# Kernel tuning notes

Measured on AMD Instinct MI355X. Metric: run time of the kernel, lower is better.

## Reference

```python
import jax, jax.numpy as jnp
import numpy as np

N_NODES = 50000
N_EDGES = 800000


def _graph_conv(feature, W, b, src, dst, edge_w, n_nodes, activation=None):
    # DGL GraphConv, norm='both', with edge_weight.
    ones = jnp.ones((src.shape[0],), dtype=feature.dtype)
    deg_out = jnp.clip(jax.ops.segment_sum(ones, src, num_segments=n_nodes), 1.0)
    deg_in = jnp.clip(jax.ops.segment_sum(ones, dst, num_segments=n_nodes), 1.0)
    # scale src side by out-deg^-1/2, transform first (in_feats > out_feats path)
    h = (feature * (deg_out ** -0.5)[:, None]) @ W            # [N, out]
    msgs = h[src] * edge_w[:, None]                            # [E, out]
    agg = jax.ops.segment_sum(msgs, dst, num_segments=n_nodes) # [N, out]
    out = agg * (deg_in ** -0.5)[:, None] + b
    if activation is not None:
        out = activation(out)
    return out


def setup_inputs() -> dict:
    key = jax.random.key(0)
    ks = jax.random.split(key, 8)
    feature = jax.random.normal(ks[0], (N_NODES, 768), dtype=jnp.float32)
    src = jax.random.randint(ks[1], (N_EDGES,), 0, N_NODES, dtype=jnp.int32)
    dst = jax.random.randint(ks[2], (N_EDGES,), 0, N_NODES, dtype=jnp.int32)
    edge_w = jax.random.uniform(ks[3], (N_EDGES,), dtype=jnp.float32)
    W1 = jax.random.normal(ks[4], (768, 200), dtype=jnp.float32) * (768 ** -0.5)
    b1 = jnp.zeros((200,), dtype=jnp.float32)
    W2 = jax.random.normal(ks[5], (200, 20), dtype=jnp.float32) * (200 ** -0.5)
    b2 = jnp.zeros((20,), dtype=jnp.float32)
    return {"feature": feature, "src": src, "dst": dst, "edge_w": edge_w,
            "W1": W1, "b1": b1, "W2": W2, "b2": b2}


def reference(feature, src, dst, edge_w, W1, b1, W2, b2):
    n = feature.shape[0]
    # dropout layers are identity in eval mode
    h = _graph_conv(feature, W1, b1, src, dst, edge_w, n, activation=jax.nn.relu)
    out = _graph_conv(h, W2, b2, src, dst, edge_w, n)
    return out
```

## Files before the change

### kernel.cpp

```cpp
#include <hip/hip_runtime.h>

#define N_NODES 50000
#define N_EDGES 800000
#define F_IN 768
#define H1 200
#define H1P 208
#define H2 20
#define NB_SCAN 196
#define NT 13

typedef unsigned short ushort_t;
typedef __attribute__((ext_vector_type(8))) short bf16x8;
typedef __attribute__((ext_vector_type(4))) float f32x4;


__global__ __launch_bounds__(256) void k_count(const int* __restrict__ src,
                                               const int* __restrict__ dst,
                                               int* __restrict__ cnt_src,
                                               int* __restrict__ cnt_dst) {
  int i = blockIdx.x * 256 + threadIdx.x;
  if (i < N_EDGES) {
    atomicAdd(&cnt_src[src[i]], 1);
    atomicAdd(&cnt_dst[dst[i]], 1);
  }
}

__global__ __launch_bounds__(256) void k_scan_block(const int* __restrict__ cnt_dst,
                                                    int* __restrict__ row_start,
                                                    int* __restrict__ partials) {
  __shared__ int sm[256];
  int i = blockIdx.x * 256 + threadIdx.x;
  int v = (i < N_NODES) ? cnt_dst[i] : 0;
  sm[threadIdx.x] = v;
  __syncthreads();
#pragma unroll
  for (int off = 1; off < 256; off <<= 1) {
    int t = (threadIdx.x >= off) ? sm[threadIdx.x - off] : 0;
    __syncthreads();
    sm[threadIdx.x] += t;
    __syncthreads();
  }
  if (i < N_NODES) row_start[i] = sm[threadIdx.x] - v;
  if (threadIdx.x == 255) partials[blockIdx.x] = sm[255];
}

__global__ __launch_bounds__(256) void k_scan_partials(int* __restrict__ partials) {
  __shared__ int sm[256];
  int v = (threadIdx.x < NB_SCAN) ? partials[threadIdx.x] : 0;
  sm[threadIdx.x] = v;
  __syncthreads();
#pragma unroll
  for (int off = 1; off < 256; off <<= 1) {
    int t = (threadIdx.x >= off) ? sm[threadIdx.x - off] : 0;
    __syncthreads();
    sm[threadIdx.x] += t;
    __syncthreads();
  }
  partials[threadIdx.x] = sm[threadIdx.x] - v;
}

__global__ __launch_bounds__(256) void k_scan_add(const int* __restrict__ cnt_dst,
                                                  const int* __restrict__ cnt_src,
                                                  const int* __restrict__ partials,
                                                  int* __restrict__ row_start,
                                                  float* __restrict__ dinv_in,
                                                  float* __restrict__ dinv_out) {
  int i = blockIdx.x * 256 + threadIdx.x;
  if (i < N_NODES) {
    row_start[i] += partials[blockIdx.x];
    dinv_in[i] = rsqrtf(fmaxf((float)cnt_dst[i], 1.f));
    dinv_out[i] = rsqrtf(fmaxf((float)cnt_src[i], 1.f));
  }
}

__global__ __launch_bounds__(256) void k_fill(const int* __restrict__ src,
                                              const int* __restrict__ dst,
                                              const float* __restrict__ ew,
                                              const int* __restrict__ row_start,
                                              int* __restrict__ cursor,
                                              int* __restrict__ src_s,
                                              float* __restrict__ w_s) {
  int e = blockIdx.x * 256 + threadIdx.x;
  if (e < N_EDGES) {
    int d = dst[e];
    int pos = atomicAdd(&cursor[d], 1);
    int idx = row_start[d] + pos;
    src_s[idx] = src[e];
    w_s[idx] = ew[e];
  }
}

__global__ __launch_bounds__(256) void k_splitW(const float* __restrict__ W1,
                                                ushort_t* __restrict__ WH,
                                                ushort_t* __restrict__ WL) {
  int idx = blockIdx.x * 256 + threadIdx.x;
  if (idx >= 208 * F_IN) return;
  int col = idx / F_IN, k = idx % F_IN;
  float f = (col < H1) ? W1[k * H1 + col] : 0.f;
  unsigned b = __float_as_uint(f);
  unsigned h = b >> 16;
  float lo = f - __uint_as_float(h << 16);
  WH[idx] = (ushort_t)h;
  WL[idx] = (ushort_t)(__float_as_uint(lo) >> 16);
}

__global__ __launch_bounds__(256) void k_gemm1_mfma(
    const float* __restrict__ A,
    const ushort_t* __restrict__ BH,
    const ushort_t* __restrict__ BL,
    const float* __restrict__ dinv_out,
    float* __restrict__ H) {
  __shared__ ushort_t AsH[64][32];
  __shared__ ushort_t AsL[64][32];
  __shared__ ushort_t BsH[NT][16][32];
  __shared__ ushort_t BsL[NT][16][32];

  const int t = threadIdx.x;
  const int wid = t >> 6;
  const int lane = t & 63;
  const int bm = blockIdx.x * 64;

  const int arow = t >> 2;
  const int akq = t & 3;
  const int aslot = (akq + ((arow >> 1) & 3)) & 3;
  const int agr = bm + arow;
  const float* __restrict__ arowp = &A[(size_t)agr * F_IN + akq * 8];

  const int frow = lane & 15;
  const int kq = lane >> 4;
  const int row_local = wid * 16 + frow;
  const int arslot = (kq + ((row_local >> 1) & 3)) & 3;
  const int brslot = (kq + ((frow >> 1) & 3)) & 3;

  const int bf = lane >> 2;
  const int bq = ((lane & 3) - ((lane >> 3) & 3)) & 3;

  f32x4 acc[NT];
#pragma unroll
  for (int i = 0; i < NT; ++i) acc[i] = (f32x4)(0.f);

  const float4 fz = make_float4(0.f, 0.f, 0.f, 0.f);
  float4 v0 = fz, v1 = fz;
  if (agr < N_NODES) {
    v0 = *(const float4*)&arowp[0];
    v1 = *(const float4*)&arowp[4];
  }

  for (int k0 = 0; k0 < F_IN; k0 += 32) {
    float fv[8] = {v0.x, v0.y, v0.z, v0.w, v1.x, v1.y, v1.z, v1.w};
    unsigned hp[4], lp[4];
#pragma unroll
    for (int i = 0; i < 4; ++i) {
      unsigned b0 = __float_as_uint(fv[2 * i]);
      unsigned b1 = __float_as_uint(fv[2 * i + 1]);
      unsigned h0 = b0 >> 16, h1 = b1 >> 16;
      float lo0 = fv[2 * i] - __uint_as_float(h0 << 16);
      float lo1 = fv[2 * i + 1] - __uint_as_float(h1 << 16);
      hp[i] = h0 | (h1 << 16);
      lp[i] = (__float_as_uint(lo0) >> 16) | (__float_as_uint(lo1) & 0xffff0000u);
    }

    __syncthreads();

    *(uint4*)&AsH[arow][aslot * 8] = make_uint4(hp[0], hp[1], hp[2], hp[3]);
    *(uint4*)&AsL[arow][aslot * 8] = make_uint4(lp[0], lp[1], lp[2], lp[3]);

    for (int nt = wid; nt < NT; nt += 4) {
      const ushort_t* gh = &BH[(size_t)(nt * 16 + bf) * F_IN + k0 + bq * 8];
      const ushort_t* gl = &BL[(size_t)(nt * 16 + bf) * F_IN + k0 + bq * 8];
      __builtin_amdgcn_global_load_lds(gh, &BsH[nt][0][0], 16, 0, 0);
      __builtin_amdgcn_global_load_lds(gl, &BsL[nt][0][0], 16, 0, 0);
    }

    v0 = fz;
    v1 = fz;
    if (k0 + 32 < F_IN && agr < N_NODES) {
      v0 = *(const float4*)&arowp[k0 + 32];
      v1 = *(const float4*)&arowp[k0 + 36];
    }

    __syncthreads();

    bf16x8 aH = *(const bf16x8*)&AsH[row_local][arslot * 8];
    bf16x8 aL = *(const bf16x8*)&AsL[row_local][arslot * 8];
#pragma unroll
    for (int nt = 0; nt < NT; ++nt) {
      bf16x8 bH = *(const bf16x8*)&BsH[nt][frow][brslot * 8];
      bf16x8 bL = *(const bf16x8*)&BsL[nt][frow][brslot * 8];
      acc[nt] = __builtin_amdgcn_mfma_f32_16x16x32_bf16(aH, bH, acc[nt], 0, 0, 0);
      acc[nt] = __builtin_amdgcn_mfma_f32_16x16x32_bf16(aH, bL, acc[nt], 0, 0, 0);
      acc[nt] = __builtin_amdgcn_mfma_f32_16x16x32_bf16(aL, bH, acc[nt], 0, 0, 0);
    }
  }

  const int r0 = bm + wid * 16 + kq * 4;
  float dsc[4];
#pragma unroll
  for (int r = 0; r < 4; ++r)
    dsc[r] = (r0 + r < N_NODES) ? dinv_out[r0 + r] : 0.f;
#pragma unroll
  for (int nt = 0; nt < NT; ++nt) {
    int gc = nt * 16 + frow;
#pragma unroll
    for (int r = 0; r < 4; ++r) {
      int gr = r0 + r;
      if (gr < N_NODES) H[(size_t)gr * H1P + gc] = acc[nt][r] * dsc[r];
    }
  }
}

__global__ __launch_bounds__(256) void k_layer1(
    const int* __restrict__ row_start, const int* __restrict__ cnt,
    const int* __restrict__ src_s, const float* __restrict__ w_s,
    const float* __restrict__ H, const float* __restrict__ dinv_in,
    const float* __restrict__ dinv_out, const float* __restrict__ b1,
    const float* __restrict__ W2, float* __restrict__ G) {
  __shared__ float Tsm[4][H1];
  const int wid = threadIdx.x >> 6;
  const int lane = threadIdx.x & 63;
  const int node = __builtin_amdgcn_readfirstlane(blockIdx.x * 4 + wid);
  const int start = __builtin_amdgcn_readfirstlane(row_start[node]);
  const int n = __builtin_amdgcn_readfirstlane(cnt[node]);
  const float4* __restrict__ Hv = (const float4*)H;
  const bool act = lane < (H1 / 4);
  float4 acc = make_float4(0.f, 0.f, 0.f, 0.f);

  int e = 0;
  for (; e + 2 <= n; e += 2) {
    int s0 = src_s[start + e];
    int s1 = src_s[start + e + 1];
    float w0 = w_s[start + e];
    float w1 = w_s[start + e + 1];
    if (act) {
      float4 u0 = Hv[(size_t)s0 * (H1P / 4) + lane];
      float4 u1 = Hv[(size_t)s1 * (H1P / 4) + lane];
      acc.x = fmaf(w0, u0.x, acc.x);
      acc.y = fmaf(w0, u0.y, acc.y);
      acc.z = fmaf(w0, u0.z, acc.z);
      acc.w = fmaf(w0, u0.w, acc.w);
      acc.x = fmaf(w1, u1.x, acc.x);
      acc.y = fmaf(w1, u1.y, acc.y);
      acc.z = fmaf(w1, u1.z, acc.z);
      acc.w = fmaf(w1, u1.w, acc.w);
    }
  }
  if (e < n) {
    int s0 = src_s[start + e];
    float w0 = w_s[start + e];
    if (act) {
      float4 u0 = Hv[(size_t)s0 * (H1P / 4) + lane];
      acc.x = fmaf(w0, u0.x, acc.x);
      acc.y = fmaf(w0, u0.y, acc.y);
      acc.z = fmaf(w0, u0.z, acc.z);
      acc.w = fmaf(w0, u0.w, acc.w);
    }
  }

  if (act) {
    float di = dinv_in[node];
    float dn = dinv_out[node];
    float4 bb = ((const float4*)b1)[lane];
    float4 r;
    r.x = fmaxf(fmaf(acc.x, di, bb.x), 0.f) * dn;
    r.y = fmaxf(fmaf(acc.y, di, bb.y), 0.f) * dn;
    r.z = fmaxf(fmaf(acc.z, di, bb.z), 0.f) * dn;
    r.w = fmaxf(fmaf(acc.w, di, bb.w), 0.f) * dn;
    *(float4*)&Tsm[wid][lane * 4] = r;
  }
  __syncthreads();

  if (lane < H2) {
    float a = 0.f;
#pragma unroll 8
    for (int d = 0; d < H1; ++d) a = fmaf(Tsm[wid][d], W2[d * H2 + lane], a);
    G[node * H2 + lane] = a;
  }
}

__global__ __launch_bounds__(256) void k_agg2_final(
    const int* __restrict__ row_start, const int* __restrict__ cnt,
    const int* __restrict__ src_s, const float* __restrict__ w_s,
    const float* __restrict__ G, const float* __restrict__ dinv_in,
    const float* __restrict__ b2, float* __restrict__ out) {
  int gi = blockIdx.x * 256 + threadIdx.x;
  if (gi >= N_NODES * H2) return;
  int node = gi / H2;
  int dim = gi % H2;
  int start = row_start[node];
  int n = cnt[node];
  float acc = 0.f;
  int e = 0;
  for (; e + 2 <= n; e += 2) {
    int s0 = src_s[start + e];
    int s1 = src_s[start + e + 1];
    float w0 = w_s[start + e];
    float w1 = w_s[start + e + 1];
    float g0 = G[s0 * H2 + dim];
    float g1 = G[s1 * H2 + dim];
    acc = fmaf(w0, g0, acc);
    acc = fmaf(w1, g1, acc);
  }
  if (e < n) {
    int s0 = src_s[start + e];
    acc = fmaf(w_s[start + e], G[s0 * H2 + dim], acc);
  }
  out[gi] = fmaf(acc, dinv_in[node], b2[dim]);
}

extern "C" void kernel_launch(void* const* d_in, const int* in_sizes, int n_in,
                              void* d_out, int out_size, void* d_ws, size_t ws_size,
                              hipStream_t stream) {
  const float* feature = (const float*)d_in[0];
  const int* src = (const int*)d_in[1];
  const int* dst = (const int*)d_in[2];
  const float* edge_w = (const float*)d_in[3];
  const float* W1 = (const float*)d_in[4];
  const float* b1 = (const float*)d_in[5];
  const float* W2 = (const float*)d_in[6];
  const float* b2 = (const float*)d_in[7];
  float* out = (float*)d_out;

  char* wsb = (char*)d_ws;
  int* cnt_dst = (int*)(wsb + 0);
  int* cnt_src = (int*)(wsb + 200000);
  int* cursor = (int*)(wsb + 400000);
  int* partials = (int*)(wsb + 600000);
  int* row_start = (int*)(wsb + 601024);
  float* dinv_in = (float*)(wsb + 801024);
  float* dinv_out = (float*)(wsb + 1001024);
  int* src_s = (int*)(wsb + 1201024);
  float* w_s = (float*)(wsb + 4401024);
  float* h = (float*)(wsb + 7601024);
  float* g2 = (float*)(wsb + 49201024);
  ushort_t* W1sH = (ushort_t*)(wsb + 53201024);
  ushort_t* W1sL = (ushort_t*)(wsb + 53520512);

  hipMemsetAsync(wsb, 0, 600000, stream);

  k_count<<<(N_EDGES + 255) / 256, 256, 0, stream>>>(src, dst, cnt_src, cnt_dst);
  k_scan_block<<<NB_SCAN, 256, 0, stream>>>(cnt_dst, row_start, partials);
  k_scan_partials<<<1, 256, 0, stream>>>(partials);
  k_scan_add<<<NB_SCAN, 256, 0, stream>>>(cnt_dst, cnt_src, partials, row_start,
                                          dinv_in, dinv_out);
  k_fill<<<(N_EDGES + 255) / 256, 256, 0, stream>>>(src, dst, edge_w, row_start,
                                                    cursor, src_s, w_s);
  k_splitW<<<(208 * F_IN + 255) / 256, 256, 0, stream>>>(W1, W1sH, W1sL);

  k_gemm1_mfma<<<(N_NODES + 63) / 64, 256, 0, stream>>>(feature, W1sH, W1sL,
                                                        dinv_out, h);

  k_layer1<<<N_NODES / 4, 256, 0, stream>>>(row_start, cnt_dst, src_s, w_s, h,
                                            dinv_in, dinv_out, b1, W2, g2);
  k_agg2_final<<<(N_NODES * H2 + 255) / 256, 256, 0, stream>>>(
      row_start, cnt_dst, src_s, w_s, g2, dinv_in, b2, out);
}
```

Before: 582.8 us.

## Load A fragments directly into registers and double K-step to 64 in GEMM1

The first-layer MFMA GEMM no longer stages the split-bf16 A tile through LDS. Each lane loads its own A row segment straight from global memory into MFMA operand registers. The K step per iteration grows from 32 to 64, halving the number of loop iterations and barrier pairs, and the B tiles are widened with a new swizzle. This removes A LDS writes and reads and some synchronisation, at the cost of more registers and less coalesced A global loads.

Result: faster. 549.0 us (-5.8%).

```diff
diff --git a/kernel.cpp b/kernel.cpp
--- a/kernel.cpp
+++ b/kernel.cpp
@@ -110,86 +110,98 @@
     const ushort_t* __restrict__ BL,
     const float* __restrict__ dinv_out,
     float* __restrict__ H) {
-  __shared__ ushort_t AsH[64][32];
-  __shared__ ushort_t AsL[64][32];
-  __shared__ ushort_t BsH[NT][16][32];
-  __shared__ ushort_t BsL[NT][16][32];
+  __shared__ ushort_t BsH[NT][16][64];
+  __shared__ ushort_t BsL[NT][16][64];
 
   const int t = threadIdx.x;
   const int wid = t >> 6;
   const int lane = t & 63;
   const int bm = blockIdx.x * 64;
 
-  const int arow = t >> 2;
-  const int akq = t & 3;
-  const int aslot = (akq + ((arow >> 1) & 3)) & 3;
-  const int agr = bm + arow;
-  const float* __restrict__ arowp = &A[(size_t)agr * F_IN + akq * 8];
-
   const int frow = lane & 15;
   const int kq = lane >> 4;
-  const int row_local = wid * 16 + frow;
-  const int arslot = (kq + ((row_local >> 1) & 3)) & 3;
-  const int brslot = (kq + ((frow >> 1) & 3)) & 3;
-
-  const int bf = lane >> 2;
-  const int bq = ((lane & 3) - ((lane >> 3) & 3)) & 3;
+  const int agr = bm + wid * 16 + frow;
+  const bool ok = agr < N_NODES;
+  const float* __restrict__ ap = &A[(size_t)agr * F_IN + kq * 8];
+
+  const int brow = lane >> 3;
+  const int bq = ((lane & 7) - brow) & 7;
+
+  const int p0 = ((kq + frow) & 7) * 8;
+  const int p1 = ((kq + 4 + frow) & 7) * 8;
 
   f32x4 acc[NT];
 #pragma unroll
   for (int i = 0; i < NT; ++i) acc[i] = (f32x4)(0.f);
 
   const float4 fz = make_float4(0.f, 0.f, 0.f, 0.f);
-  float4 v0 = fz, v1 = fz;
-  if (agr < N_NODES) {
-    v0 = *(const float4*)&arowp[0];
-    v1 = *(const float4*)&arowp[4];
-  }
-
-  for (int k0 = 0; k0 < F_IN; k0 += 32) {
-    float fv[8] = {v0.x, v0.y, v0.z, v0.w, v1.x, v1.y, v1.z, v1.w};
-    unsigned hp[4], lp[4];
-#pragma unroll
-    for (int i = 0; i < 4; ++i) {
+  float4 c0 = fz, c1 = fz, c2 = fz, c3 = fz;
+  if (ok) {
+    c0 = *(const float4*)(ap + 0);
+    c1 = *(const float4*)(ap + 4);
+    c2 = *(const float4*)(ap + 32);
+    c3 = *(const float4*)(ap + 36);
+  }
+
+  for (int k0 = 0; k0 < F_IN; k0 += 64) {
+    float fv[16] = {c0.x, c0.y, c0.z, c0.w, c1.x, c1.y, c1.z, c1.w,
+                    c2.x, c2.y, c2.z, c2.w, c3.x, c3.y, c3.z, c3.w};
+    unsigned hp[8], lp[8];
+#pragma unroll
+    for (int i = 0; i < 8; ++i) {
       unsigned b0 = __float_as_uint(fv[2 * i]);
       unsigned b1 = __float_as_uint(fv[2 * i + 1]);
       unsigned h0 = b0 >> 16, h1 = b1 >> 16;
-      float lo0 = fv[2 * i] - __uint_as_float(h0 << 16);
-      float lo1 = fv[2 * i + 1] - __uint_as_float(h1 << 16);
+      float l0 = fv[2 * i] - __uint_as_float(h0 << 16);
+      float l1 = fv[2 * i + 1] - __uint_as_float(h1 << 16);
       hp[i] = h0 | (h1 << 16);
-      lp[i] = (__float_as_uint(lo0) >> 16) | (__float_as_uint(lo1) & 0xffff0000u);
-    }
-
-    __syncthreads();
-
-    *(uint4*)&AsH[arow][aslot * 8] = make_uint4(hp[0], hp[1], hp[2], hp[3]);
-    *(uint4*)&AsL[arow][aslot * 8] = make_uint4(lp[0], lp[1], lp[2], lp[3]);
+      lp[i] = (__float_as_uint(l0) >> 16) | (__float_as_uint(l1) & 0xffff0000u);
+    }
+    uint4 uH0 = make_uint4(hp[0], hp[1], hp[2], hp[3]);
+    uint4 uL0 = make_uint4(lp[0], lp[1], lp[2], lp[3]);
+    uint4 uH1 = make_uint4(hp[4], hp[5], hp[6], hp[7]);
+    uint4 uL1 = make_uint4(lp[4], lp[5], lp[6], lp[7]);
+    bf16x8 aH0 = *(bf16x8*)&uH0;
+    bf16x8 aL0 = *(bf16x8*)&uL0;
+    bf16x8 aH1 = *(bf16x8*)&uH1;
+    bf16x8 aL1 = *(bf16x8*)&uL1;
+
+    __syncthreads();
 
     for (int nt = wid; nt < NT; nt += 4) {
-      const ushort_t* gh = &BH[(size_t)(nt * 16 + bf) * F_IN + k0 + bq * 8];
-      const ushort_t* gl = &BL[(size_t)(nt * 16 + bf) * F_IN + k0 + bq * 8];
-      __builtin_amdgcn_global_load_lds(gh, &BsH[nt][0][0], 16, 0, 0);
-      __builtin_amdgcn_global_load_lds(gl, &BsL[nt][0][0], 16, 0, 0);
-    }
-
-    v0 = fz;
-    v1 = fz;
-    if (k0 + 32 < F_IN && agr < N_NODES) {
-      v0 = *(const float4*)&arowp[k0 + 32];
-      v1 = *(const float4*)&arowp[k0 + 36];
-    }
-
-    __syncthreads();
-
-    bf16x8 aH = *(const bf16x8*)&AsH[row_local][arslot * 8];
-    bf16x8 aL = *(const bf16x8*)&AsL[row_local][arslot * 8];
+#pragma unroll
+      for (int h2 = 0; h2 < 2; ++h2) {
+        const ushort_t* gh =
+            &BH[(size_t)(nt * 16 + h2 * 8 + brow) * F_IN + k0 + bq * 8];
+        const ushort_t* gl =
+            &BL[(size_t)(nt * 16 + h2 * 8 + brow) * F_IN + k0 + bq * 8];
+        __builtin_amdgcn_global_load_lds(gh, &BsH[nt][h2 * 8][0], 16, 0, 0);
+        __builtin_amdgcn_global_load_lds(gl, &BsL[nt][h2 * 8][0], 16, 0, 0);
+      }
+    }
+
+    c0 = fz; c1 = fz; c2 = fz; c3 = fz;
+    if (k0 + 64 < F_IN && ok) {
+      c0 = *(const float4*)(ap + k0 + 64);
+      c1 = *(const float4*)(ap + k0 + 68);
+      c2 = *(const float4*)(ap + k0 + 96);
+      c3 = *(const float4*)(ap + k0 + 100);
+    }
+
+    __syncthreads();
+
 #pragma unroll
     for (int nt = 0; nt < NT; ++nt) {
-      bf16x8 bH = *(const bf16x8*)&BsH[nt][frow][brslot * 8];
-      bf16x8 bL = *(const bf16x8*)&BsL[nt][frow][brslot * 8];
-      acc[nt] = __builtin_amdgcn_mfma_f32_16x16x32_bf16(aH, bH, acc[nt], 0, 0, 0);
-      acc[nt] = __builtin_amdgcn_mfma_f32_16x16x32_bf16(aH, bL, acc[nt], 0, 0, 0);
-      acc[nt] = __builtin_amdgcn_mfma_f32_16x16x32_bf16(aL, bH, acc[nt], 0, 0, 0);
+      bf16x8 bH0 = *(const bf16x8*)&BsH[nt][frow][p0];
+      bf16x8 bL0 = *(const bf16x8*)&BsL[nt][frow][p0];
+      bf16x8 bH1 = *(const bf16x8*)&BsH[nt][frow][p1];
+      bf16x8 bL1 = *(const bf16x8*)&BsL[nt][frow][p1];
+      acc[nt] = __builtin_amdgcn_mfma_f32_16x16x32_bf16(aH0, bH0, acc[nt], 0, 0, 0);
+      acc[nt] = __builtin_amdgcn_mfma_f32_16x16x32_bf16(aH0, bL0, acc[nt], 0, 0, 0);
+      acc[nt] = __builtin_amdgcn_mfma_f32_16x16x32_bf16(aL0, bH0, acc[nt], 0, 0, 0);
+      acc[nt] = __builtin_amdgcn_mfma_f32_16x16x32_bf16(aH1, bH1, acc[nt], 0, 0, 0);
+      acc[nt] = __builtin_amdgcn_mfma_f32_16x16x32_bf16(aH1, bL1, acc[nt], 0, 0, 0);
+      acc[nt] = __builtin_amdgcn_mfma_f32_16x16x32_bf16(aL1, bH1, acc[nt], 0, 0, 0);
     }
   }
 
```
